# Optimization experiments

Hardware: AMD Instinct MI355X
Metric: run time of the kernel (lower is better)

Reference implementation:

```python
import jax, jax.numpy as jnp
import numpy as np

B, T, D = 2, 2048, 1024
H = 16
HD = D // H          # 64
WIN = 512            # sliding window size


def _band_mask(t, win):
    i = jnp.arange(t)[:, None]
    j = jnp.arange(t)[None, :]
    return ((j <= i) & (j > i - win)).astype(jnp.float32)


def setup_inputs() -> dict:
    key = jax.random.key(0)
    ks = jax.random.split(key, 7)
    s = 0.02
    return {
        "x":  jax.random.normal(ks[0], (B, T, D), dtype=jnp.float32),
        "Wg": jax.random.normal(ks[1], (D, D), dtype=jnp.float32) * s,
        "bg": jnp.zeros((D,), dtype=jnp.float32),
        "Wv": jax.random.normal(ks[2], (D, H * HD), dtype=jnp.float32) * s,
        "bv": jnp.zeros((H * HD,), dtype=jnp.float32),
        "Wo": jax.random.normal(ks[3], (D, D), dtype=jnp.float32) * s,
        "bo": jnp.zeros((D,), dtype=jnp.float32),
    }


def genetic_fitness(pop, mask):
    # pop: (B,H,T,D_head); mask: (T,T)
    # gene_means[b,h,i,d] = sum_j mask[i,j]*pop[b,h,j,d] / active_counts[i]
    counts = jnp.maximum(mask.sum(axis=1), 1.0)                 # (T,)
    gene_means = jnp.einsum('ij,bhjd->bhid', mask, pop) / counts[None, None, :, None]
    denom = gene_means + 0.5                                    # (B,H,T,Dh)
    sum_inv = (1.0 / denom).sum(axis=-1, keepdims=True)
    gene_fit = 1.0 / (denom * sum_inv)                          # (B,H,T,Dh)
    # org_fitness[b,h,i,j] = mask[i,j] * <gene_fit[b,h,i], pop[b,h,j]>
    org = mask[None, None] * jnp.einsum('bhid,bhjd->bhij', gene_fit, pop)
    row = jnp.maximum(org.sum(axis=-1, keepdims=True), 1e-10)
    return org / row                                            # (B,H,T,T)


def reference(x, Wg, bg, Wv, bv, Wo, bo):
    mask = _band_mask(T, WIN)
    g = (x @ Wg + bg).reshape(B, T, H, HD).transpose(0, 2, 1, 3)   # (B,H,T,Dh)
    v = (x @ Wv + bv).reshape(B, T, H, HD).transpose(0, 2, 1, 3)   # (B,H,T,Dh)
    attn = genetic_fitness(g, mask)                                 # (B,H,T,T)
    out = jnp.einsum('bhij,bhjd->bhid', attn, v)                    # (B,H,T,Dh)
    out = out.transpose(0, 2, 1, 3).reshape(B, T, D)
    return out @ Wo + bo
```

## Files before the change

### kernel.cpp

```cpp
#include <hip/hip_runtime.h>

#define NB 2
#define NT 2048
#define ND 1024
#define NH 16
#define HD 64
#define WIN 512
#define NBH (NB*NH)
#define NCH (NT/64)

typedef short    bf16x8 __attribute__((ext_vector_type(8)));
typedef unsigned short us8 __attribute__((ext_vector_type(8)));
typedef unsigned short us4 __attribute__((ext_vector_type(4)));
typedef float    f32x4  __attribute__((ext_vector_type(4)));

__device__ __forceinline__ void split_bf16(float f, unsigned short& h, unsigned short& l)
{
    unsigned u = __float_as_uint(f);
    h = (unsigned short)(u >> 16);
    float fh = __uint_as_float(u & 0xffff0000u);
    l = (unsigned short)(__float_as_uint(f - fh) >> 16);
}

__device__ __forceinline__ unsigned short bf_rne(float f)
{
    unsigned u = __float_as_uint(f);
    u += 0x7fffu + ((u >> 16) & 1u);
    return (unsigned short)(u >> 16);
}

__device__ __forceinline__ void split3(float f, unsigned short& h,
                                       unsigned short& m, unsigned short& l)
{
    h = bf_rne(f);
    const float fh = __uint_as_float((unsigned)h << 16);
    const float r1 = f - fh;
    m = bf_rne(r1);
    const float fm = __uint_as_float((unsigned)m << 16);
    const float r2 = r1 - fm;
    l = bf_rne(r2);
}

__device__ __forceinline__ us8 pack8(float4 a, float4 b)
{
    us8 r;
    r[0] = bf_rne(a.x); r[1] = bf_rne(a.y); r[2] = bf_rne(a.z); r[3] = bf_rne(a.w);
    r[4] = bf_rne(b.x); r[5] = bf_rne(b.y); r[6] = bf_rne(b.z); r[7] = bf_rne(b.w);
    return r;
}

__global__ __launch_bounds__(256)
void mgemm3_k(const unsigned short* __restrict__ Ah, const unsigned short* __restrict__ Am,
              const unsigned short* __restrict__ Al,
              const unsigned short* __restrict__ Bh, const unsigned short* __restrict__ Bm,
              const unsigned short* __restrict__ Bl,
              const float* __restrict__ bias, float* __restrict__ C,
              int M, int N, int K)
{
    __shared__ unsigned short As[3][128 * 32];
    __shared__ unsigned short Bs[3][128 * 32];
    const int tid = threadIdx.x;
    const int wave = tid >> 6, lane = tid & 63;
    const int wm = wave >> 1, wn = wave & 1;
    const int m0 = blockIdx.y << 7, n0 = blockIdx.x << 7;
    const int l15 = lane & 15;

    const int srow = tid >> 1, skh = tid & 1;
    const int ssw = (srow & 3) ^ ((srow >> 2) & 3);
    const int sA0 = srow * 32 + ((((skh << 1) | 0) ^ ssw) << 3);
    const int sA1 = srow * 32 + ((((skh << 1) | 1) ^ ssw) << 3);
    const size_t aoff = (size_t)(m0 + srow) * K + (skh << 4);
    const size_t boff = (size_t)(n0 + srow) * K + (skh << 4);

    us8 a0[2], a1[2], a2[2], b0[2], b1[2], b2[2];
    a0[0] = *(const us8*)(Ah + aoff); a0[1] = *(const us8*)(Ah + aoff + 8);
    a1[0] = *(const us8*)(Am + aoff); a1[1] = *(const us8*)(Am + aoff + 8);
    a2[0] = *(const us8*)(Al + aoff); a2[1] = *(const us8*)(Al + aoff + 8);
    b0[0] = *(const us8*)(Bh + boff); b0[1] = *(const us8*)(Bh + boff + 8);
    b1[0] = *(const us8*)(Bm + boff); b1[1] = *(const us8*)(Bm + boff + 8);
    b2[0] = *(const us8*)(Bl + boff); b2[1] = *(const us8*)(Bl + boff + 8);

    const int fsw = ((lane >> 4) ^ (lane & 3) ^ ((lane & 12) >> 2)) << 3;

    f32x4 acc[4][4] = {};
    for (int k0 = 0; k0 < K; k0 += 32) {
        __syncthreads();
        *(us8*)&As[0][sA0] = a0[0]; *(us8*)&As[0][sA1] = a0[1];
        *(us8*)&As[1][sA0] = a1[0]; *(us8*)&As[1][sA1] = a1[1];
        *(us8*)&As[2][sA0] = a2[0]; *(us8*)&As[2][sA1] = a2[1];
        *(us8*)&Bs[0][sA0] = b0[0]; *(us8*)&Bs[0][sA1] = b0[1];
        *(us8*)&Bs[1][sA0] = b1[0]; *(us8*)&Bs[1][sA1] = b1[1];
        *(us8*)&Bs[2][sA0] = b2[0]; *(us8*)&Bs[2][sA1] = b2[1];
        __syncthreads();
        if (k0 + 32 < K) {
            const size_t ka = aoff + k0 + 32, kb = boff + k0 + 32;
            a0[0] = *(const us8*)(Ah + ka); a0[1] = *(const us8*)(Ah + ka + 8);
            a1[0] = *(const us8*)(Am + ka); a1[1] = *(const us8*)(Am + ka + 8);
            a2[0] = *(const us8*)(Al + ka); a2[1] = *(const us8*)(Al + ka + 8);
            b0[0] = *(const us8*)(Bh + kb); b0[1] = *(const us8*)(Bh + kb + 8);
            b1[0] = *(const us8*)(Bm + kb); b1[1] = *(const us8*)(Bm + kb + 8);
            b2[0] = *(const us8*)(Bl + kb); b2[1] = *(const us8*)(Bl + kb + 8);
        }
        bf16x8 aF[3][4], bF[3][4];
#pragma unroll
        for (int s = 0; s < 4; ++s) {
            const int ra = (wm << 6) + (s << 4) + l15;
            const int rb = (wn << 6) + (s << 4) + l15;
#pragma unroll
            for (int p = 0; p < 3; ++p) {
                aF[p][s] = *(const bf16x8*)&As[p][ra * 32 + fsw];
                bF[p][s] = *(const bf16x8*)&Bs[p][rb * 32 + fsw];
            }
        }
#pragma unroll
        for (int ms = 0; ms < 4; ++ms)
#pragma unroll
            for (int ns = 0; ns < 4; ++ns) {
                f32x4 t = acc[ms][ns];
                t = __builtin_amdgcn_mfma_f32_16x16x32_bf16(aF[0][ms], bF[0][ns], t, 0, 0, 0);
                t = __builtin_amdgcn_mfma_f32_16x16x32_bf16(aF[0][ms], bF[1][ns], t, 0, 0, 0);
                t = __builtin_amdgcn_mfma_f32_16x16x32_bf16(aF[1][ms], bF[0][ns], t, 0, 0, 0);
                t = __builtin_amdgcn_mfma_f32_16x16x32_bf16(aF[0][ms], bF[2][ns], t, 0, 0, 0);
                t = __builtin_amdgcn_mfma_f32_16x16x32_bf16(aF[2][ms], bF[0][ns], t, 0, 0, 0);
                t = __builtin_amdgcn_mfma_f32_16x16x32_bf16(aF[1][ms], bF[1][ns], t, 0, 0, 0);
                acc[ms][ns] = t;
            }
    }

#pragma unroll
    for (int ms = 0; ms < 4; ++ms)
#pragma unroll
        for (int ns = 0; ns < 4; ++ns) {
            const int col = n0 + (wn << 6) + (ns << 4) + l15;
            const float bb = bias[col];
            const int h = col >> 6, d = col & 63;
#pragma unroll
            for (int r = 0; r < 4; ++r) {
                const int row = m0 + (wm << 6) + (ms << 4) + ((lane >> 4) << 2) + r;
                const int b = row >> 11, i = row & (NT - 1);
                C[((((size_t)(b * NH + h)) << 11) + i) * HD + d] = acc[ms][ns][r] + bb;
            }
        }
}

template<int MODE>
__global__ __launch_bounds__(256)
void mgemm_k(const unsigned short* __restrict__ Ahi, const unsigned short* __restrict__ Alo,
             const unsigned short* __restrict__ Bhi, const unsigned short* __restrict__ Blo,
             const float* __restrict__ bias, float* __restrict__ C,
             int M, int N, int K)
{
    __shared__ unsigned short As[2][128 * 32];
    __shared__ unsigned short Bs[2][128 * 32];
    const int tid = threadIdx.x;
    const int wave = tid >> 6, lane = tid & 63;
    const int wm = wave >> 1, wn = wave & 1;
    const int m0 = blockIdx.y << 7, n0 = blockIdx.x << 7;

    const int srow = tid >> 1, skh = tid & 1;
    const int ssw = (srow & 3) ^ ((srow >> 2) & 3);
    const int sA0 = srow * 32 + ((((skh << 1) | 0) ^ ssw) << 3);
    const int sA1 = srow * 32 + ((((skh << 1) | 1) ^ ssw) << 3);
    const size_t aoff = (size_t)(m0 + srow) * K + (skh << 4);
    const size_t boff = (size_t)(n0 + srow) * K + (skh << 4);

    us8 ah0 = *(const us8*)(Ahi + aoff), ah1 = *(const us8*)(Ahi + aoff + 8);
    us8 al0 = *(const us8*)(Alo + aoff), al1 = *(const us8*)(Alo + aoff + 8);
    us8 bh0 = *(const us8*)(Bhi + boff), bh1 = *(const us8*)(Bhi + boff + 8);
    us8 bl0 = *(const us8*)(Blo + boff), bl1 = *(const us8*)(Blo + boff + 8);

    const int fsw = ((lane >> 4) ^ (lane & 3) ^ ((lane & 12) >> 2)) << 3;

    f32x4 acc[4][4] = {};
    for (int k0 = 0; k0 < K; k0 += 32) {
        __syncthreads();
        *(us8*)&As[0][sA0] = ah0; *(us8*)&As[0][sA1] = ah1;
        *(us8*)&As[1][sA0] = al0; *(us8*)&As[1][sA1] = al1;
        *(us8*)&Bs[0][sA0] = bh0; *(us8*)&Bs[0][sA1] = bh1;
        *(us8*)&Bs[1][sA0] = bl0; *(us8*)&Bs[1][sA1] = bl1;
        __syncthreads();
        if (k0 + 32 < K) {
            const size_t ka = aoff + k0 + 32, kb = boff + k0 + 32;
            ah0 = *(const us8*)(Ahi + ka); ah1 = *(const us8*)(Ahi + ka + 8);
            al0 = *(const us8*)(Alo + ka); al1 = *(const us8*)(Alo + ka + 8);
            bh0 = *(const us8*)(Bhi + kb); bh1 = *(const us8*)(Bhi + kb + 8);
            bl0 = *(const us8*)(Blo + kb); bl1 = *(const us8*)(Blo + kb + 8);
        }
        bf16x8 aH[4], aL[4], bH[4], bL[4];
#pragma unroll
        for (int s = 0; s < 4; ++s) {
            const int ra = (wm << 6) + (s << 4) + (lane & 15);
            const int rb = (wn << 6) + (s << 4) + (lane & 15);
            aH[s] = *(const bf16x8*)&As[0][ra * 32 + fsw];
            aL[s] = *(const bf16x8*)&As[1][ra * 32 + fsw];
            bH[s] = *(const bf16x8*)&Bs[0][rb * 32 + fsw];
            bL[s] = *(const bf16x8*)&Bs[1][rb * 32 + fsw];
        }
#pragma unroll
        for (int ms = 0; ms < 4; ++ms)
#pragma unroll
            for (int ns = 0; ns < 4; ++ns) {
                acc[ms][ns] = __builtin_amdgcn_mfma_f32_16x16x32_bf16(aH[ms], bH[ns], acc[ms][ns], 0, 0, 0);
                acc[ms][ns] = __builtin_amdgcn_mfma_f32_16x16x32_bf16(aH[ms], bL[ns], acc[ms][ns], 0, 0, 0);
                acc[ms][ns] = __builtin_amdgcn_mfma_f32_16x16x32_bf16(aL[ms], bH[ns], acc[ms][ns], 0, 0, 0);
            }
    }

#pragma unroll
    for (int ms = 0; ms < 4; ++ms)
#pragma unroll
        for (int ns = 0; ns < 4; ++ns) {
            const int col = n0 + (wn << 6) + (ns << 4) + (lane & 15);
            const float bb = bias[col];
#pragma unroll
            for (int r = 0; r < 4; ++r) {
                const int row = m0 + (wm << 6) + (ms << 4) + ((lane >> 4) << 2) + r;
                const float val = acc[ms][ns][r] + bb;
                if (MODE == 0) {
                    C[(size_t)row * N + col] = val;
                } else {
                    const int b = row >> 11, i = row & (NT - 1);
                    const int h = col >> 6;
                    C[((((size_t)(b * NH + h)) << 11) + i) * HD + (col & 63)] = val;
                }
            }
        }
}

__global__ __launch_bounds__(256)
void split3_k(const float* __restrict__ x, unsigned short* __restrict__ xh,
              unsigned short* __restrict__ xm, unsigned short* __restrict__ xl)
{
    const int e0 = (blockIdx.x * 256 + threadIdx.x) << 2;
    const float4 v = *(const float4*)&x[e0];
    ushort4 hh, mm, ll;
    split3(v.x, hh.x, mm.x, ll.x); split3(v.y, hh.y, mm.y, ll.y);
    split3(v.z, hh.z, mm.z, ll.z); split3(v.w, hh.w, mm.w, ll.w);
    *(ushort4*)&xh[e0] = hh;
    *(ushort4*)&xm[e0] = mm;
    *(ushort4*)&xl[e0] = ll;
}

__global__ __launch_bounds__(256)
void tsplit_k(const float* __restrict__ W, unsigned short* __restrict__ Th,
              unsigned short* __restrict__ Tl)
{
    __shared__ float Ls[64][68];
    const int n0 = blockIdx.x << 6, k0 = blockIdx.y << 6;
    const int tid = threadIdx.x;
    const int r16 = tid >> 4, c4 = (tid & 15) << 2;
#pragma unroll
    for (int j = 0; j < 4; ++j) {
        const int row = r16 + (j << 4);
        *(float4*)&Ls[row][c4] = *(const float4*)&W[(size_t)(k0 + row) * ND + n0 + c4];
    }
    __syncthreads();
#pragma unroll
    for (int j = 0; j < 4; ++j) {
        const int n = r16 + (j << 4);
        ushort4 hh, ll;
        split_bf16(Ls[c4 + 0][n], hh.x, ll.x);
        split_bf16(Ls[c4 + 1][n], hh.y, ll.y);
        split_bf16(Ls[c4 + 2][n], hh.z, ll.z);
        split_bf16(Ls[c4 + 3][n], hh.w, ll.w);
        const size_t o = (size_t)(n0 + n) * ND + k0 + c4;
        *(ushort4*)&Th[o] = hh;
        *(ushort4*)&Tl[o] = ll;
    }
}

__global__ __launch_bounds__(256)
void tsplit3_k(const float* __restrict__ W, unsigned short* __restrict__ T0,
               unsigned short* __restrict__ T1, unsigned short* __restrict__ T2)
{
    __shared__ float Ls[64][68];
    const int n0 = blockIdx.x << 6, k0 = blockIdx.y << 6;
    const int tid = threadIdx.x;
    const int r16 = tid >> 4, c4 = (tid & 15) << 2;
#pragma unroll
    for (int j = 0; j < 4; ++j) {
        const int row = r16 + (j << 4);
        *(float4*)&Ls[row][c4] = *(const float4*)&W[(size_t)(k0 + row) * ND + n0 + c4];
    }
    __syncthreads();
#pragma unroll
    for (int j = 0; j < 4; ++j) {
        const int n = r16 + (j << 4);
        ushort4 hh, mm, ll;
        split3(Ls[c4 + 0][n], hh.x, mm.x, ll.x);
        split3(Ls[c4 + 1][n], hh.y, mm.y, ll.y);
        split3(Ls[c4 + 2][n], hh.z, mm.z, ll.z);
        split3(Ls[c4 + 3][n], hh.w, mm.w, ll.w);
        const size_t o = (size_t)(n0 + n) * ND + k0 + c4;
        *(ushort4*)&T0[o] = hh;
        *(ushort4*)&T1[o] = mm;
        *(ushort4*)&T2[o] = ll;
    }
}

__global__ __launch_bounds__(64)
void chunkscan_k(const float* __restrict__ g, float* __restrict__ Pin,
                 float* __restrict__ Csum)
{
    const int blk = blockIdx.x;
    const int lane = threadIdx.x;
    const int base = (blk << 12) + lane;
    float run = 0.f;
#pragma unroll 16
    for (int t = 0; t < 64; ++t) {
        run += g[base + (t << 6)];
        Pin[base + (t << 6)] = run;
    }
    Csum[(blk << 6) + lane] = run;
}

__global__ __launch_bounds__(64)
void chunkpre_k(const float* __restrict__ Csum, float* __restrict__ Cpre)
{
    const int bh = blockIdx.x, lane = threadIdx.x;
    float run = 0.f;
    for (int c = 0; c < NCH; ++c) {
        run += Csum[((bh * NCH + c) << 6) + lane];
        Cpre[((bh * NCH + c) << 6) + lane] = run;
    }
}

__global__ __launch_bounds__(256)
void winsum_k(const float* __restrict__ Pin, const float* __restrict__ Cpre,
              float* __restrict__ wout)
{
    const int idx = blockIdx.x * 256 + threadIdx.x;
    const int e0 = idx << 2;
    const int row = e0 >> 6;
    const int d = e0 & 63;
    const int bh = row >> 11;
    const int i = row & (NT - 1);
    const int c = i >> 6;

    float4 p = *(const float4*)&Pin[e0];
    float ax = p.x, ay = p.y, az = p.z, aw = p.w;
    if (c > 0) {
        const float4 q = *(const float4*)&Cpre[((bh * NCH + c - 1) << 6) + d];
        ax += q.x; ay += q.y; az += q.z; aw += q.w;
    }
    if (i >= WIN) {
        const int i2 = i - WIN;
        const int c2 = i2 >> 6;
        const float4 p2 = *(const float4*)&Pin[(((bh << 11) + i2) << 6) + d];
        ax -= p2.x; ay -= p2.y; az -= p2.z; aw -= p2.w;
        if (c2 > 0) {
            const float4 q2 = *(const float4*)&Cpre[((bh * NCH + c2 - 1) << 6) + d];
            ax -= q2.x; ay -= q2.y; az -= q2.z; aw -= q2.w;
        }
    }
    *(float4*)&wout[e0] = make_float4(ax, ay, az, aw);
}

__global__ __launch_bounds__(256)
void stats_k(float* __restrict__ wing, double* __restrict__ rowsum)
{
    const int row = (blockIdx.x << 2) + (threadIdx.x >> 6);
    const int lane = threadIdx.x & 63;
    const int i = row & (NT - 1);
    const float w = wing[(row << 6) + lane];
    const double cnt = (double)((i + 1 < WIN) ? (i + 1) : WIN);
    const double denom = (double)w / cnt + 0.5;
    double s = 1.0 / denom;
#pragma unroll
    for (int off = 32; off > 0; off >>= 1) s += __shfl_xor(s, off);
    const double gf = 1.0 / (denom * s);
    double rw = gf * (double)w;
#pragma unroll
    for (int off = 32; off > 0; off >>= 1) rw += __shfl_xor(rw, off);
    wing[(row << 6) + lane] = (float)gf;
    if (lane == 0) rowsum[row] = rw;
}

__global__ __launch_bounds__(256)
void attn_k(const float* __restrict__ gf, const float* __restrict__ g,
            const float* __restrict__ v, const double* __restrict__ rowsum,
            unsigned short* __restrict__ aoh, unsigned short* __restrict__ aol)
{
    __shared__ unsigned short gL[64 * 72];
    __shared__ unsigned short VT[64 * 72];
    __shared__ unsigned short SL[64 * 72];

    const int bh = blockIdx.y, it = blockIdx.x;
    const int i0 = it << 6;
    const int tid = threadIdx.x;
    const int wave = tid >> 6, lane = tid & 63;
    const int l15 = lane & 15, l4 = lane >> 4;

    bf16x8 gfB[2];
    {
        const int ig = i0 + (wave << 4) + l15;
        const float* src = gf + (((size_t)(bh << 11) + ig) << 6) + (l4 << 3);
        const float4 q0 = *(const float4*)(src);
        const float4 q1 = *(const float4*)(src + 4);
        const float4 q2 = *(const float4*)(src + 32);
        const float4 q3 = *(const float4*)(src + 36);
        const us8 f0 = pack8(q0, q1), f1 = pack8(q2, q3);
        gfB[0] = (bf16x8)f0;
        gfB[1] = (bf16x8)f1;
    }

    const int sj = lane, sd0 = wave << 4;

    const int t_lo = (it >= 8) ? (it - 8) : 0;
    float4 gq[4], vq[4];
    {
        const float* gsrc = g + (((size_t)(bh << 11) + (t_lo << 6) + sj) << 6) + sd0;
        const float* vsrc = v + (((size_t)(bh << 11) + (t_lo << 6) + sj) << 6) + sd0;
#pragma unroll
        for (int q = 0; q < 4; ++q) gq[q] = *(const float4*)(gsrc + (q << 2));
#pragma unroll
        for (int q = 0; q < 4; ++q) vq[q] = *(const float4*)(vsrc + (q << 2));
    }

    f32x4 acc2[4] = {};
    const int ig_mask = i0 + (wave << 4) + l15;

    for (int t = t_lo; t <= it; ++t) {
        const int j0 = t << 6;
        __syncthreads();
        {
            *(us8*)&gL[sj * 72 + sd0]     = pack8(gq[0], gq[1]);
            *(us8*)&gL[sj * 72 + sd0 + 8] = pack8(gq[2], gq[3]);
            const float* vf = (const float*)vq;
#pragma unroll
            for (int h = 0; h < 16; ++h)
                VT[(sd0 + h) * 72 + sj] = bf_rne(vf[h]);
        }
        __syncthreads();

        if (t < it) {
            const float* gsrc = g + (((size_t)(bh << 11) + j0 + 64 + sj) << 6) + sd0;
            const float* vsrc = v + (((size_t)(bh << 11) + j0 + 64 + sj) << 6) + sd0;
#pragma unroll
            for (int q = 0; q < 4; ++q) gq[q] = *(const float4*)(gsrc + (q << 2));
#pragma unroll
            for (int q = 0; q < 4; ++q) vq[q] = *(const float4*)(vsrc + (q << 2));
        }

        f32x4 sfr[4] = {};
#pragma unroll
        for (int kk = 0; kk < 2; ++kk)
#pragma unroll
            for (int jm = 0; jm < 4; ++jm) {
                const bf16x8 ag = *(const bf16x8*)&gL[((jm << 4) + l15) * 72 + (kk << 5) + (l4 << 3)];
                sfr[jm] = __builtin_amdgcn_mfma_f32_16x16x32_bf16(ag, gfB[kk], sfr[jm], 0, 0, 0);
            }

        const bool need_mask = (t == it) || (t == it - 8);
#pragma unroll
        for (int jm = 0; jm < 4; ++jm) {
            float s0 = sfr[jm][0], s1 = sfr[jm][1], s2 = sfr[jm][2], s3 = sfr[jm][3];
            if (need_mask) {
                const int jb = j0 + (jm << 4) + (l4 << 2);
                if (!(jb + 0 <= ig_mask && jb + 0 > ig_mask - WIN)) s0 = 0.f;
                if (!(jb + 1 <= ig_mask && jb + 1 > ig_mask - WIN)) s1 = 0.f;
                if (!(jb + 2 <= ig_mask && jb + 2 > ig_mask - WIN)) s2 = 0.f;
                if (!(jb + 3 <= ig_mask && jb + 3 > ig_mask - WIN)) s3 = 0.f;
            }
            us4 sl;
            sl[0] = bf_rne(s0); sl[1] = bf_rne(s1); sl[2] = bf_rne(s2); sl[3] = bf_rne(s3);
            *(us4*)&SL[((wave << 4) + l15) * 72 + (jm << 4) + (l4 << 2)] = sl;
        }

#pragma unroll
        for (int kk = 0; kk < 2; ++kk) {
            const bf16x8 a2 = *(const bf16x8*)&SL[((wave << 4) + l15) * 72 + (kk << 5) + (l4 << 3)];
#pragma unroll
            for (int nf = 0; nf < 4; ++nf) {
                const bf16x8 b2 = *(const bf16x8*)&VT[((nf << 4) + l15) * 72 + (kk << 5) + (l4 << 3)];
                acc2[nf] = __builtin_amdgcn_mfma_f32_16x16x32_bf16(a2, b2, acc2[nf], 0, 0, 0);
            }
        }
    }

    const int b = bh >> 4, hh = bh & 15;
    float inv[4];
#pragma unroll
    for (int r = 0; r < 4; ++r) {
        const int ig = i0 + (wave << 4) + (l4 << 2) + r;
        double rs = rowsum[(bh << 11) + ig];
        if (!(rs > 1e-10)) rs = 1e-10;
        inv[r] = (float)(1.0 / rs);
    }
#pragma unroll
    for (int nf = 0; nf < 4; ++nf)
#pragma unroll
        for (int r = 0; r < 4; ++r) {
            const int ig = i0 + (wave << 4) + (l4 << 2) + r;
            const int d = (nf << 4) + l15;
            const float val = acc2[nf][r] * inv[r];
            unsigned short vh, vl;
            split_bf16(val, vh, vl);
            const size_t base = (((size_t)(b * NT + ig)) << 10) + (hh << 6) + d;
            aoh[base] = vh;
            aol[base] = vl;
        }
}

extern "C" void kernel_launch(void* const* d_in, const int* in_sizes, int n_in,
                              void* d_out, int out_size, void* d_ws, size_t ws_size,
                              hipStream_t stream)
{
    const float* x  = (const float*)d_in[0];
    const float* Wg = (const float*)d_in[1];
    const float* bg = (const float*)d_in[2];
    const float* Wv = (const float*)d_in[3];
    const float* bv = (const float*)d_in[4];
    const float* Wo = (const float*)d_in[5];
    const float* bo = (const float*)d_in[6];
    float* out = (float*)d_out;

    const size_t SZ = (size_t)NB * NH * NT * HD;
    const size_t MW = (size_t)ND * ND;
    const size_t CS = (size_t)NBH * NCH * HD;

    float* gbuf = (float*)d_ws;
    float* vbuf = gbuf + SZ;
    float* pinb = vbuf + SZ;
    float* winb = pinb + SZ;
    float* wpl  = winb + SZ;

    unsigned short* wvTh = (unsigned short*)wpl;
    unsigned short* wvTl = wvTh + MW;
    unsigned short* woTh = wvTl + MW;
    unsigned short* woTl = woTh + MW;
    unsigned short* wgT0 = woTl + MW;
    unsigned short* wgT1 = wgT0 + MW;
    unsigned short* wgT2 = wgT1 + MW;

    float* csum = (float*)wgT0;
    float* cpre = csum + CS;
    double* rsum = (double*)(cpre + CS);

    unsigned short* xh  = (unsigned short*)winb;
    unsigned short* xm  = xh + SZ;
    unsigned short* xl  = (unsigned short*)pinb;
    unsigned short* aoh = (unsigned short*)pinb;
    unsigned short* aol = aoh + SZ;

    const int M = NB * NT;

    split3_k<<<(int)(SZ / 4 / 256), 256, 0, stream>>>(x, xh, xm, xl);
    tsplit3_k<<<dim3(ND >> 6, ND >> 6), 256, 0, stream>>>(Wg, wgT0, wgT1, wgT2);
    tsplit_k<<<dim3(ND >> 6, ND >> 6), 256, 0, stream>>>(Wv, wvTh, wvTl);
    tsplit_k<<<dim3(ND >> 6, ND >> 6), 256, 0, stream>>>(Wo, woTh, woTl);
    mgemm3_k<<<dim3(ND >> 7, M >> 7), 256, 0, stream>>>(xh, xm, xl, wgT0, wgT1, wgT2, bg, gbuf, M, ND, ND);
    mgemm_k<1><<<dim3(ND >> 7, M >> 7), 256, 0, stream>>>(xh, xm, wvTh, wvTl, bv, vbuf, M, ND, ND);
    chunkscan_k<<<NBH * NCH, 64, 0, stream>>>(gbuf, pinb, csum);
    chunkpre_k<<<NBH, 64, 0, stream>>>(csum, cpre);
    winsum_k<<<(NBH * NT * HD / 4) / 256, 256, 0, stream>>>(pinb, cpre, winb);
    stats_k<<<(NBH * NT) / 4, 256, 0, stream>>>(winb, rsum);
    attn_k<<<dim3(NT >> 6, NBH), 256, 0, stream>>>(winb, gbuf, vbuf, rsum, aoh, aol);
    mgemm_k<0><<<dim3(ND >> 7, M >> 7), 256, 0, stream>>>(aoh, aol, woTh, woTl, bo, out, M, ND, ND);
}
```

Before: 340.7 us.

## Double-buffer LDS in split-bf16 GEMMs and remap tiles across XCDs

Both split-precision GEMM kernels move from a single LDS buffer with two barriers per k-step to double-buffered LDS with one barrier per step. The next tile is stored into the alternate buffer while MFMAs run on the current one, and global loads are issued two steps ahead. A new xcd_tile mapping reorders block indices so neighbouring M tiles land on the same XCD, aiming at better L2 reuse. The cost is doubled LDS use (the 3-plane kernel reaches 96KB), which may cut occupancy, and the mapping hardcodes an 8-wide grid, so it is only correct for grids of that shape.

Result: faster. 333.7 us (-2.0%).

```diff
diff --git a/kernel.cpp b/kernel.cpp
--- a/kernel.cpp
+++ b/kernel.cpp
@@ -49,6 +49,29 @@
     return r;
 }
 
+__device__ __forceinline__ void xcd_tile(int& m0, int& n0)
+{
+    const int s = blockIdx.y * 8 + blockIdx.x;
+    const int c = s & 7, r = s >> 3;
+    m0 = ((c << 2) | (r & 3)) << 7;
+    n0 = (r >> 2) << 7;
+}
+
+#define LOADT3(koff) { const size_t ka = aoff + (koff), kb = boff + (koff);            \
+    a0[0]=*(const us8*)(Ah+ka); a0[1]=*(const us8*)(Ah+ka+8);                          \
+    a1[0]=*(const us8*)(Am+ka); a1[1]=*(const us8*)(Am+ka+8);                          \
+    a2[0]=*(const us8*)(Al+ka); a2[1]=*(const us8*)(Al+ka+8);                          \
+    b0[0]=*(const us8*)(Bh+kb); b0[1]=*(const us8*)(Bh+kb+8);                          \
+    b1[0]=*(const us8*)(Bm+kb); b1[1]=*(const us8*)(Bm+kb+8);                          \
+    b2[0]=*(const us8*)(Bl+kb); b2[1]=*(const us8*)(Bl+kb+8); }
+#define STORET3(buf) {                                                                  \
+    *(us8*)&As[buf][0][sA0]=a0[0]; *(us8*)&As[buf][0][sA1]=a0[1];                      \
+    *(us8*)&As[buf][1][sA0]=a1[0]; *(us8*)&As[buf][1][sA1]=a1[1];                      \
+    *(us8*)&As[buf][2][sA0]=a2[0]; *(us8*)&As[buf][2][sA1]=a2[1];                      \
+    *(us8*)&Bs[buf][0][sA0]=b0[0]; *(us8*)&Bs[buf][0][sA1]=b0[1];                      \
+    *(us8*)&Bs[buf][1][sA0]=b1[0]; *(us8*)&Bs[buf][1][sA1]=b1[1];                      \
+    *(us8*)&Bs[buf][2][sA0]=b2[0]; *(us8*)&Bs[buf][2][sA1]=b2[1]; }
+
 __global__ __launch_bounds__(256)
 void mgemm3_k(const unsigned short* __restrict__ Ah, const unsigned short* __restrict__ Am,
               const unsigned short* __restrict__ Al,
@@ -57,12 +80,13 @@
               const float* __restrict__ bias, float* __restrict__ C,
               int M, int N, int K)
 {
-    __shared__ unsigned short As[3][128 * 32];
-    __shared__ unsigned short Bs[3][128 * 32];
+    __shared__ unsigned short As[2][3][128 * 32];
+    __shared__ unsigned short Bs[2][3][128 * 32];
     const int tid = threadIdx.x;
     const int wave = tid >> 6, lane = tid & 63;
     const int wm = wave >> 1, wn = wave & 1;
-    const int m0 = blockIdx.y << 7, n0 = blockIdx.x << 7;
+    int m0, n0;
+    xcd_tile(m0, n0);
     const int l15 = lane & 15;
 
     const int srow = tid >> 1, skh = tid & 1;
@@ -73,34 +97,16 @@
     const size_t boff = (size_t)(n0 + srow) * K + (skh << 4);
 
     us8 a0[2], a1[2], a2[2], b0[2], b1[2], b2[2];
-    a0[0] = *(const us8*)(Ah + aoff); a0[1] = *(const us8*)(Ah + aoff + 8);
-    a1[0] = *(const us8*)(Am + aoff); a1[1] = *(const us8*)(Am + aoff + 8);
-    a2[0] = *(const us8*)(Al + aoff); a2[1] = *(const us8*)(Al + aoff + 8);
-    b0[0] = *(const us8*)(Bh + boff); b0[1] = *(const us8*)(Bh + boff + 8);
-    b1[0] = *(const us8*)(Bm + boff); b1[1] = *(const us8*)(Bm + boff + 8);
-    b2[0] = *(const us8*)(Bl + boff); b2[1] = *(const us8*)(Bl + boff + 8);
+    LOADT3(0);
+    STORET3(0);
+    LOADT3(32);
+    __syncthreads();
 
     const int fsw = ((lane >> 4) ^ (lane & 3) ^ ((lane & 12) >> 2)) << 3;
 
     f32x4 acc[4][4] = {};
     for (int k0 = 0; k0 < K; k0 += 32) {
-        __syncthreads();
-        *(us8*)&As[0][sA0] = a0[0]; *(us8*)&As[0][sA1] = a0[1];
-        *(us8*)&As[1][sA0] = a1[0]; *(us8*)&As[1][sA1] = a1[1];
-        *(us8*)&As[2][sA0] = a2[0]; *(us8*)&As[2][sA1] = a2[1];
-        *(us8*)&Bs[0][sA0] = b0[0]; *(us8*)&Bs[0][sA1] = b0[1];
-        *(us8*)&Bs[1][sA0] = b1[0]; *(us8*)&Bs[1][sA1] = b1[1];
-        *(us8*)&Bs[2][sA0] = b2[0]; *(us8*)&Bs[2][sA1] = b2[1];
-        __syncthreads();
-        if (k0 + 32 < K) {
-            const size_t ka = aoff + k0 + 32, kb = boff + k0 + 32;
-            a0[0] = *(const us8*)(Ah + ka); a0[1] = *(const us8*)(Ah + ka + 8);
-            a1[0] = *(const us8*)(Am + ka); a1[1] = *(const us8*)(Am + ka + 8);
-            a2[0] = *(const us8*)(Al + ka); a2[1] = *(const us8*)(Al + ka + 8);
-            b0[0] = *(const us8*)(Bh + kb); b0[1] = *(const us8*)(Bh + kb + 8);
-            b1[0] = *(const us8*)(Bm + kb); b1[1] = *(const us8*)(Bm + kb + 8);
-            b2[0] = *(const us8*)(Bl + kb); b2[1] = *(const us8*)(Bl + kb + 8);
-        }
+        const int cur = (k0 >> 5) & 1;
         bf16x8 aF[3][4], bF[3][4];
 #pragma unroll
         for (int s = 0; s < 4; ++s) {
@@ -108,10 +114,12 @@
             const int rb = (wn << 6) + (s << 4) + l15;
 #pragma unroll
             for (int p = 0; p < 3; ++p) {
-                aF[p][s] = *(const bf16x8*)&As[p][ra * 32 + fsw];
-                bF[p][s] = *(const bf16x8*)&Bs[p][rb * 32 + fsw];
-            }
-        }
+                aF[p][s] = *(const bf16x8*)&As[cur][p][ra * 32 + fsw];
+                bF[p][s] = *(const bf16x8*)&Bs[cur][p][rb * 32 + fsw];
+            }
+        }
+        if (k0 + 32 < K) STORET3(cur ^ 1);
+        if (k0 + 64 < K) LOADT3(k0 + 64);
 #pragma unroll
         for (int ms = 0; ms < 4; ++ms)
 #pragma unroll
@@ -125,6 +133,7 @@
                 t = __builtin_amdgcn_mfma_f32_16x16x32_bf16(aF[1][ms], bF[1][ns], t, 0, 0, 0);
                 acc[ms][ns] = t;
             }
+        __syncthreads();
     }
 
 #pragma unroll
@@ -143,6 +152,17 @@
         }
 }
 
+#define LOADT2(koff) { const size_t ka = aoff + (koff), kb = boff + (koff);            \
+    ah0=*(const us8*)(Ahi+ka); ah1=*(const us8*)(Ahi+ka+8);                            \
+    al0=*(const us8*)(Alo+ka); al1=*(const us8*)(Alo+ka+8);                            \
+    bh0=*(const us8*)(Bhi+kb); bh1=*(const us8*)(Bhi+kb+8);                            \
+    bl0=*(const us8*)(Blo+kb); bl1=*(const us8*)(Blo+kb+8); }
+#define STORET2(buf) {                                                                  \
+    *(us8*)&As[buf][0][sA0]=ah0; *(us8*)&As[buf][0][sA1]=ah1;                          \
+    *(us8*)&As[buf][1][sA0]=al0; *(us8*)&As[buf][1][sA1]=al1;                          \
+    *(us8*)&Bs[buf][0][sA0]=bh0; *(us8*)&Bs[buf][0][sA1]=bh1;                          \
+    *(us8*)&Bs[buf][1][sA0]=bl0; *(us8*)&Bs[buf][1][sA1]=bl1; }
+
 template<int MODE>
 __global__ __launch_bounds__(256)
 void mgemm_k(const unsigned short* __restrict__ Ahi, const unsigned short* __restrict__ Alo,
@@ -150,12 +170,14 @@
              const float* __restrict__ bias, float* __restrict__ C,
              int M, int N, int K)
 {
-    __shared__ unsigned short As[2][128 * 32];
-    __shared__ unsigned short Bs[2][128 * 32];
+    __shared__ unsigned short As[2][2][128 * 32];
+    __shared__ unsigned short Bs[2][2][128 * 32];
     const int tid = threadIdx.x;
     const int wave = tid >> 6, lane = tid & 63;
     const int wm = wave >> 1, wn = wave & 1;
-    const int m0 = blockIdx.y << 7, n0 = blockIdx.x << 7;
+    int m0, n0;
+    xcd_tile(m0, n0);
+    const int l15 = lane & 15;
 
     const int srow = tid >> 1, skh = tid & 1;
     const int ssw = (srow & 3) ^ ((srow >> 2) & 3);
@@ -164,38 +186,29 @@
     const size_t aoff = (size_t)(m0 + srow) * K + (skh << 4);
     const size_t boff = (size_t)(n0 + srow) * K + (skh << 4);
 
-    us8 ah0 = *(const us8*)(Ahi + aoff), ah1 = *(const us8*)(Ahi + aoff + 8);
-    us8 al0 = *(const us8*)(Alo + aoff), al1 = *(const us8*)(Alo + aoff + 8);
-    us8 bh0 = *(const us8*)(Bhi + boff), bh1 = *(const us8*)(Bhi + boff + 8);
-    us8 bl0 = *(const us8*)(Blo + boff), bl1 = *(const us8*)(Blo + boff + 8);
+    us8 ah0, ah1, al0, al1, bh0, bh1, bl0, bl1;
+    LOADT2(0);
+    STORET2(0);
+    LOADT2(32);
+    __syncthreads();
 
     const int fsw = ((lane >> 4) ^ (lane & 3) ^ ((lane & 12) >> 2)) << 3;
 
     f32x4 acc[4][4] = {};
     for (int k0 = 0; k0 < K; k0 += 32) {
-        __syncthreads();
-        *(us8*)&As[0][sA0] = ah0; *(us8*)&As[0][sA1] = ah1;
-        *(us8*)&As[1][sA0] = al0; *(us8*)&As[1][sA1] = al1;
-        *(us8*)&Bs[0][sA0] = bh0; *(us8*)&Bs[0][sA1] = bh1;
-        *(us8*)&Bs[1][sA0] = bl0; *(us8*)&Bs[1][sA1] = bl1;
-        __syncthreads();
-        if (k0 + 32 < K) {
-            const size_t ka = aoff + k0 + 32, kb = boff + k0 + 32;
-            ah0 = *(const us8*)(Ahi + ka); ah1 = *(const us8*)(Ahi + ka + 8);
-            al0 = *(const us8*)(Alo + ka); al1 = *(const us8*)(Alo + ka + 8);
-            bh0 = *(const us8*)(Bhi + kb); bh1 = *(const us8*)(Bhi + kb + 8);
-            bl0 = *(const us8*)(Blo + kb); bl1 = *(const us8*)(Blo + kb + 8);
-        }
+        const int cur = (k0 >> 5) & 1;
         bf16x8 aH[4], aL[4], bH[4], bL[4];
 #pragma unroll
         for (int s = 0; s < 4; ++s) {
-            const int ra = (wm << 6) + (s << 4) + (lane & 15);
-            const int rb = (wn << 6) + (s << 4) + (lane & 15);
-            aH[s] = *(const bf16x8*)&As[0][ra * 32 + fsw];
-            aL[s] = *(const bf16x8*)&As[1][ra * 32 + fsw];
-            bH[s] = *(const bf16x8*)&Bs[0][rb * 32 + fsw];
-            bL[s] = *(const bf16x8*)&Bs[1][rb * 32 + fsw];
-        }
+            const int ra = (wm << 6) + (s << 4) + l15;
+            const int rb = (wn << 6) + (s << 4) + l15;
+            aH[s] = *(const bf16x8*)&As[cur][0][ra * 32 + fsw];
+            aL[s] = *(const bf16x8*)&As[cur][1][ra * 32 + fsw];
+            bH[s] = *(const bf16x8*)&Bs[cur][0][rb * 32 + fsw];
+            bL[s] = *(const bf16x8*)&Bs[cur][1][rb * 32 + fsw];
+        }
+        if (k0 + 32 < K) STORET2(cur ^ 1);
+        if (k0 + 64 < K) LOADT2(k0 + 64);
 #pragma unroll
         for (int ms = 0; ms < 4; ++ms)
 #pragma unroll
@@ -204,13 +217,14 @@
                 acc[ms][ns] = __builtin_amdgcn_mfma_f32_16x16x32_bf16(aH[ms], bL[ns], acc[ms][ns], 0, 0, 0);
                 acc[ms][ns] = __builtin_amdgcn_mfma_f32_16x16x32_bf16(aL[ms], bH[ns], acc[ms][ns], 0, 0, 0);
             }
+        __syncthreads();
     }
 
 #pragma unroll
     for (int ms = 0; ms < 4; ++ms)
 #pragma unroll
         for (int ns = 0; ns < 4; ++ns) {
-            const int col = n0 + (wn << 6) + (ns << 4) + (lane & 15);
+            const int col = n0 + (wn << 6) + (ns << 4) + l15;
             const float bb = bias[col];
 #pragma unroll
             for (int r = 0; r < 4; ++r) {
```
